# Kernel tuning notes

Measured on AMD Instinct MI355X. Metric: run time of the kernel, lower is better.

## Reference

```python
import jax, jax.numpy as jnp
import numpy as np

N = 100000   # nodes
E = 1600000  # edges
D = 128      # in_dim == hidden_dim
EL = 100000  # label edges for decode


def setup_inputs() -> dict:
    key = jax.random.key(0)
    k1, k2, k3, k4, k5 = jax.random.split(key, 5)
    x = jax.random.normal(k1, (N, D), dtype=jnp.float32)
    edge_index = jax.random.randint(k2, (2, E), 0, N, dtype=jnp.int64)
    edge_label_index = jax.random.randint(k3, (2, EL), 0, N, dtype=jnp.int64)
    # Glorot-ish init for GCN weights
    scale = 1.0 / np.sqrt(D)
    W1 = jax.random.normal(k4, (D, D), dtype=jnp.float32) * scale
    W2 = jax.random.normal(k5, (D, D), dtype=jnp.float32) * scale
    b1 = jnp.zeros((D,), dtype=jnp.float32)
    b2 = jnp.zeros((D,), dtype=jnp.float32)
    return {"x": x, "edge_index": edge_index, "edge_label_index": edge_label_index,
            "W1": W1, "b1": b1, "W2": W2, "b2": b2}


def gcn_conv(x, src, dst, W, b, num_nodes):
    # PyG GCNConv: add self-loops, symmetric D^-1/2 A D^-1/2 normalization
    loop = jnp.arange(num_nodes, dtype=src.dtype)
    s = jnp.concatenate([src, loop])
    d = jnp.concatenate([dst, loop])
    deg = jax.ops.segment_sum(jnp.ones(d.shape, dtype=x.dtype), d, num_segments=num_nodes)
    dinv = jnp.where(deg > 0, jax.lax.rsqrt(jnp.maximum(deg, 1.0)), 0.0)
    norm = dinv[s] * dinv[d]                      # [E+N]
    h = x @ W                                     # [N, H]
    msg = h[s] * norm[:, None]                    # gather + scale
    out = jax.ops.segment_sum(msg, d, num_segments=num_nodes)  # scatter-add
    return out + b


def reference(x, edge_index, edge_label_index, W1, b1, W2, b2):
    src, dst = edge_index[0], edge_index[1]
    z = jax.nn.relu(gcn_conv(x, src, dst, W1, b1, N))
    z = jax.nn.relu(gcn_conv(z, src, dst, W2, b2, N))
    # decode: edge-wise dot product
    s, d = edge_label_index[0], edge_label_index[1]
    return jnp.sum(z[s] * z[d], axis=-1)          # [EL]
```

## Files before the change

### kernel.cpp

```cpp
#include <hip/hip_runtime.h>
#include <hip/hip_bf16.h>
#include <hip/hip_fp16.h>


typedef _Float16 half8 __attribute__((ext_vector_type(8)));
typedef float floatx4 __attribute__((ext_vector_type(4)));

#define BK_SHIFT 8
#define BSC_EDGES 2048
#define SLAB_CAP 5120
#define WPAD 136

__global__ __launch_bounds__(256) void k_zero(int* __restrict__ p, int n) {
    int i = blockIdx.x * 256 + threadIdx.x;
    if (i < n) p[i] = 0;
}

__global__ __launch_bounds__(128) void k_wprep(const float* __restrict__ W1,
                                               const float* __restrict__ W2,
                                               _Float16* __restrict__ WT1,
                                               _Float16* __restrict__ WT2) {
    int b = blockIdx.x;
    const float* W = (b < 128) ? W1 : W2;
    _Float16* WT = (b < 128) ? WT1 : WT2;
    int k = b & 127;
    int c = threadIdx.x;
    WT[c * 128 + k] = (_Float16)W[k * 128 + c];
}

__global__ __launch_bounds__(256) void k_bscatter(const int* __restrict__ src,
                                                  const int* __restrict__ dst,
                                                  int* __restrict__ bfill,
                                                  int2* __restrict__ pairs,
                                                  int E, int nbk) {
    __shared__ int lcnt[1024];
    __shared__ int delta[1024];
    __shared__ int ssum[256];
    __shared__ int2 stage[BSC_EDGES];
    int tid = threadIdx.x;
    int e0 = blockIdx.x * BSC_EDGES;
    int nloc = E - e0; if (nloc > BSC_EDGES) nloc = BSC_EDGES;

    for (int b = tid; b < nbk; b += 256) lcnt[b] = 0;
    __syncthreads();

    int d[BSC_EDGES / 256], s[BSC_EDGES / 256];
#pragma unroll
    for (int k = 0; k < BSC_EDGES / 256; ++k) {
        int e = e0 + k * 256 + tid;
        if (e < E) {
            d[k] = dst[e];
            s[k] = src[e];
            atomicAdd(&lcnt[d[k] >> BK_SHIFT], 1);
        } else d[k] = -1;
    }
    __syncthreads();

    const int gpb = (nbk + 255) >> 8;
    int c[4], mysum = 0;
    for (int t = 0; t < gpb; ++t) {
        int b = tid * gpb + t;
        c[t] = (b < nbk) ? lcnt[b] : 0;
        mysum += c[t];
    }
    ssum[tid] = mysum;
    __syncthreads();
    for (int off = 1; off < 256; off <<= 1) {
        int t = (tid >= off) ? ssum[tid - off] : 0;
        __syncthreads();
        ssum[tid] += t;
        __syncthreads();
    }
    int base = ssum[tid] - mysum;
    for (int t = 0; t < gpb; ++t) {
        int b = tid * gpb + t;
        if (b < nbk) {
            int g = c[t] ? atomicAdd(&bfill[b], c[t]) : 0;
            delta[b] = b * SLAB_CAP + g - base;
            lcnt[b] = base;
            base += c[t];
        }
    }
    __syncthreads();

#pragma unroll
    for (int k = 0; k < BSC_EDGES / 256; ++k) {
        if (d[k] >= 0) {
            int b = d[k] >> BK_SHIFT;
            int lp = atomicAdd(&lcnt[b], 1);
            int2 p; p.x = s[k]; p.y = d[k];
            stage[lp] = p;
        }
    }
    __syncthreads();

    for (int j = tid; j < nloc; j += 256) {
        int2 p = stage[j];
        pairs[delta[p.y >> BK_SHIFT] + j] = p;
    }
}

__global__ __launch_bounds__(256) void k_csr(const int2* __restrict__ pairs,
                                             const int* __restrict__ bfill,
                                             int* __restrict__ row_start,
                                             int* __restrict__ cnt,
                                             float* __restrict__ dinv,
                                             int* __restrict__ srcs, int n) {
    __shared__ int lcnt[256];
    __shared__ int lpos[256];
    int tid = threadIdx.x;
    int b = blockIdx.x;
    lcnt[tid] = 0;
    __syncthreads();
    int beg = b * SLAB_CAP, end = beg + bfill[b];
    for (int i = beg + tid; i < end; i += 256)
        atomicAdd(&lcnt[pairs[i].y & 255], 1);
    __syncthreads();
    int c = lcnt[tid];
    lpos[tid] = c;
    __syncthreads();
    for (int off = 1; off < 256; off <<= 1) {
        int t = (tid >= off) ? lpos[tid - off] : 0;
        __syncthreads();
        lpos[tid] += t;
        __syncthreads();
    }
    int rs = beg + lpos[tid] - c;
    int v = (b << BK_SHIFT) + tid;
    if (v < n) {
        row_start[v] = rs;
        cnt[v] = c;
        dinv[v] = rsqrtf((float)c + 1.0f);
    }
    __syncthreads();
    lpos[tid] = rs;
    __syncthreads();
    for (int i = beg + tid; i < end; i += 256) {
        int2 p = pairs[i];
        int loc = atomicAdd(&lpos[p.y & 255], 1);
        srcs[loc] = p.x;
    }
}

__global__ __launch_bounds__(256) void k_gemm_mfma(const float* __restrict__ X,
                                                   const _Float16* __restrict__ WT,
                                                   const float* __restrict__ dinv,
                                                   _Float16* __restrict__ G, int n) {
    __shared__ _Float16 Wl[128 * WPAD];
    int tid = threadIdx.x;
    {
        const half8* w8 = (const half8*)WT;
#pragma unroll
        for (int i = 0; i < 8; ++i) {
            int idx = i * 256 + tid;
            int r = idx >> 4, cc = idx & 15;
            *(half8*)(Wl + r * WPAD + cc * 8) = w8[idx];
        }
    }
    __syncthreads();

    int wave = tid >> 6, lane = tid & 63;
    int q = lane >> 4, ln = lane & 15;
    int m0 = blockIdx.x * 128 + wave * 32;
    int mA0 = m0 + ln;      if (mA0 >= n) mA0 = n - 1;
    int mA1 = m0 + 16 + ln; if (mA1 >= n) mA1 = n - 1;
    const float* xr0 = X + (size_t)mA0 * 128;
    const float* xr1 = X + (size_t)mA1 * 128;

    floatx4 acc[2][8];
#pragma unroll
    for (int p = 0; p < 2; ++p)
#pragma unroll
        for (int t = 0; t < 8; ++t) acc[p][t] = (floatx4){0.f, 0.f, 0.f, 0.f};

#pragma unroll
    for (int kc = 0; kc < 128; kc += 32) {
        half8 a0, a1;
        {
            const float4* p0 = (const float4*)(xr0 + kc + q * 8);
            float4 f0 = p0[0], f1 = p0[1];
            a0[0] = (_Float16)f0.x; a0[1] = (_Float16)f0.y;
            a0[2] = (_Float16)f0.z; a0[3] = (_Float16)f0.w;
            a0[4] = (_Float16)f1.x; a0[5] = (_Float16)f1.y;
            a0[6] = (_Float16)f1.z; a0[7] = (_Float16)f1.w;
            const float4* p1 = (const float4*)(xr1 + kc + q * 8);
            float4 g0 = p1[0], g1 = p1[1];
            a1[0] = (_Float16)g0.x; a1[1] = (_Float16)g0.y;
            a1[2] = (_Float16)g0.z; a1[3] = (_Float16)g0.w;
            a1[4] = (_Float16)g1.x; a1[5] = (_Float16)g1.y;
            a1[6] = (_Float16)g1.z; a1[7] = (_Float16)g1.w;
        }
#pragma unroll
        for (int t = 0; t < 8; ++t) {
            half8 b = *(const half8*)(Wl + (size_t)(t * 16 + ln) * WPAD + kc + q * 8);
            acc[0][t] = __builtin_amdgcn_mfma_f32_16x16x32_f16(a0, b, acc[0][t], 0, 0, 0);
            acc[1][t] = __builtin_amdgcn_mfma_f32_16x16x32_f16(a1, b, acc[1][t], 0, 0, 0);
        }
    }

#pragma unroll
    for (int p = 0; p < 2; ++p) {
#pragma unroll
        for (int r = 0; r < 4; ++r) {
            int row = m0 + p * 16 + q * 4 + r;
            if (row < n) {
                float dv = dinv[row];
                _Float16* grow = G + (size_t)row * 128 + ln;
#pragma unroll
                for (int t = 0; t < 8; ++t)
                    grow[t * 16] = (_Float16)(acc[p][t][r] * dv);
            }
        }
    }
}

__global__ __launch_bounds__(256) void k_gather_gemm(const _Float16* __restrict__ G,
                                                     const int* __restrict__ srcs,
                                                     const int* __restrict__ row_start,
                                                     const int* __restrict__ cnt,
                                                     const float* __restrict__ dinv,
                                                     const float* __restrict__ bias,
                                                     const _Float16* __restrict__ WT2,
                                                     _Float16* __restrict__ G2, int n) {
    __shared__ _Float16 Wl[128 * WPAD];
    __shared__ _Float16 zl[16 * WPAD];
    int tid = threadIdx.x;

    {
        const half8* w8 = (const half8*)WT2;
#pragma unroll
        for (int i = 0; i < 8; ++i) {
            int idx = i * 256 + tid;
            int r = idx >> 4, cc = idx & 15;
            *(half8*)(Wl + r * WPAD + cc * 8) = w8[idx];
        }
    }

    int nl = tid >> 4;
    int lane = tid & 15;
    int v = blockIdx.x * 16 + nl;
    const half8* G8 = (const half8*)G;

    half8 zo;
    if (v < n) {
        half8 self = G8[(size_t)v * 16 + lane];
        float acc[8], acc2[8];
#pragma unroll
        for (int j = 0; j < 8; ++j) { acc[j] = (float)self[j]; acc2[j] = 0.f; }

        int beg = row_start[v], deg = cnt[v];
        int e = 0;
        for (; e + 3 < deg; e += 4) {
            int s0 = srcs[beg + e];
            int s1 = srcs[beg + e + 1];
            int s2 = srcs[beg + e + 2];
            int s3 = srcs[beg + e + 3];
            half8 t0 = G8[(size_t)s0 * 16 + lane];
            half8 t1 = G8[(size_t)s1 * 16 + lane];
            half8 t2 = G8[(size_t)s2 * 16 + lane];
            half8 t3 = G8[(size_t)s3 * 16 + lane];
#pragma unroll
            for (int j = 0; j < 8; ++j) {
                acc[j]  += (float)t0[j] + (float)t1[j];
                acc2[j] += (float)t2[j] + (float)t3[j];
            }
        }
        for (; e < deg; ++e) {
            int s0 = srcs[beg + e];
            half8 t0 = G8[(size_t)s0 * 16 + lane];
#pragma unroll
            for (int j = 0; j < 8; ++j) acc[j] += (float)t0[j];
        }

        float dv = dinv[v];
        const float4* b4 = (const float4*)bias;
        float4 bb0 = b4[lane * 2], bb1 = b4[lane * 2 + 1];
        float bf[8] = {bb0.x, bb0.y, bb0.z, bb0.w, bb1.x, bb1.y, bb1.z, bb1.w};
#pragma unroll
        for (int j = 0; j < 8; ++j) {
            float z = dv * (acc[j] + acc2[j]) + bf[j];
            zo[j] = (_Float16)fmaxf(z, 0.f);
        }
    } else {
#pragma unroll
        for (int j = 0; j < 8; ++j) zo[j] = (_Float16)0.f;
    }
    *(half8*)(zl + nl * WPAD + lane * 8) = zo;
    __syncthreads();

    int wave = tid >> 6, wl = tid & 63;
    int q = wl >> 4, ln = wl & 15;
    floatx4 acc[2];
    acc[0] = (floatx4){0.f, 0.f, 0.f, 0.f};
    acc[1] = (floatx4){0.f, 0.f, 0.f, 0.f};
#pragma unroll
    for (int kc = 0; kc < 128; kc += 32) {
        half8 a = *(const half8*)(zl + ln * WPAD + kc + q * 8);
#pragma unroll
        for (int t = 0; t < 2; ++t) {
            int cb = wave * 32 + t * 16;
            half8 b = *(const half8*)(Wl + (size_t)(cb + ln) * WPAD + kc + q * 8);
            acc[t] = __builtin_amdgcn_mfma_f32_16x16x32_f16(a, b, acc[t], 0, 0, 0);
        }
    }
#pragma unroll
    for (int r = 0; r < 4; ++r) {
        int gv = blockIdx.x * 16 + q * 4 + r;
        if (gv < n) {
            float dv = dinv[gv];
#pragma unroll
            for (int t = 0; t < 2; ++t)
                G2[(size_t)gv * 128 + wave * 32 + t * 16 + ln] =
                    (_Float16)(acc[t][r] * dv);
        }
    }
}

__global__ __launch_bounds__(256) void k_gather_relu(const _Float16* __restrict__ G,
                                                     const int* __restrict__ srcs,
                                                     const int* __restrict__ row_start,
                                                     const int* __restrict__ cnt,
                                                     const float* __restrict__ dinv,
                                                     const float* __restrict__ bias,
                                                     _Float16* __restrict__ Z, int n) {
    int v = blockIdx.x * 16 + (threadIdx.x >> 4);
    int lane = threadIdx.x & 15;
    if (v >= n) return;
    const half8* G8 = (const half8*)G;

    half8 self = G8[(size_t)v * 16 + lane];
    float acc[8], acc2[8];
#pragma unroll
    for (int j = 0; j < 8; ++j) { acc[j] = (float)self[j]; acc2[j] = 0.f; }

    int beg = row_start[v], deg = cnt[v];
    int e = 0;
    for (; e + 3 < deg; e += 4) {
        int s0 = srcs[beg + e];
        int s1 = srcs[beg + e + 1];
        int s2 = srcs[beg + e + 2];
        int s3 = srcs[beg + e + 3];
        half8 t0 = G8[(size_t)s0 * 16 + lane];
        half8 t1 = G8[(size_t)s1 * 16 + lane];
        half8 t2 = G8[(size_t)s2 * 16 + lane];
        half8 t3 = G8[(size_t)s3 * 16 + lane];
#pragma unroll
        for (int j = 0; j < 8; ++j) {
            acc[j]  += (float)t0[j] + (float)t1[j];
            acc2[j] += (float)t2[j] + (float)t3[j];
        }
    }
    for (; e < deg; ++e) {
        int s0 = srcs[beg + e];
        half8 t0 = G8[(size_t)s0 * 16 + lane];
#pragma unroll
        for (int j = 0; j < 8; ++j) acc[j] += (float)t0[j];
    }

    float dv = dinv[v];
    const float4* b4 = (const float4*)bias;
    float4 bb0 = b4[lane * 2], bb1 = b4[lane * 2 + 1];
    float bf[8] = {bb0.x, bb0.y, bb0.z, bb0.w, bb1.x, bb1.y, bb1.z, bb1.w};
    half8 zo;
#pragma unroll
    for (int j = 0; j < 8; ++j) {
        float z = dv * (acc[j] + acc2[j]) + bf[j];
        zo[j] = (_Float16)fmaxf(z, 0.f);
    }
    ((half8*)Z)[(size_t)v * 16 + lane] = zo;
}

__global__ __launch_bounds__(256) void k_decode(const _Float16* __restrict__ Z,
                                                const int* __restrict__ eli,
                                                float* __restrict__ out, int el) {
    int sub = threadIdx.x >> 4, lane = threadIdx.x & 15;
    int e = blockIdx.x * 16 + sub;
    if (e >= el) return;
    int s = eli[e], d = eli[el + e];
    const half8* Z8 = (const half8*)Z;
    half8 a = Z8[(size_t)s * 16 + lane];
    half8 b = Z8[(size_t)d * 16 + lane];
    float dot = 0.f;
#pragma unroll
    for (int j = 0; j < 8; ++j) dot += (float)a[j] * (float)b[j];
#pragma unroll
    for (int off = 8; off; off >>= 1) dot += __shfl_down(dot, off, 16);
    if (lane == 0) out[e] = dot;
}

extern "C" void kernel_launch(void* const* d_in, const int* in_sizes, int n_in,
                              void* d_out, int out_size, void* d_ws, size_t ws_size,
                              hipStream_t stream) {
    const float* x  = (const float*)d_in[0];
    const int*  ei  = (const int*)d_in[1];
    const int*  eli = (const int*)d_in[2];
    const float* W1 = (const float*)d_in[3];
    const float* b1 = (const float*)d_in[4];
    const float* W2 = (const float*)d_in[5];
    const float* b2 = (const float*)d_in[6];
    float* out = (float*)d_out;

    const int N  = in_sizes[0] / 128;
    const int E  = in_sizes[1] / 2;
    const int EL = in_sizes[2] / 2;
    const int* src = ei;
    const int* dst = ei + E;
    const int NBK = (N + 255) >> BK_SHIFT;

    char* ws = (char*)d_ws;
    size_t off = 0;
    auto alloc = [&](size_t bytes) -> void* {
        void* p = ws + off;
        off += bytes;
        off = (off + 255) & ~(size_t)255;
        return p;
    };
    int*       cnt       = (int*)alloc((size_t)N * 4);
    int*       row_start = (int*)alloc((size_t)N * 4);
    float*     dinv      = (float*)alloc((size_t)N * 4);
    int*       bfill     = (int*)alloc(4096);
    _Float16*  WT1       = (_Float16*)alloc(128 * 128 * 2);
    _Float16*  WT2       = (_Float16*)alloc(128 * 128 * 2);
    int*       srcs      = (int*)alloc((size_t)NBK * SLAB_CAP * 4);
    int2*      pairs     = (int2*)alloc((size_t)NBK * SLAB_CAP * 8);
    _Float16*  buf0      = (_Float16*)alloc((size_t)N * 128 * 2);
    _Float16*  buf1      = (_Float16*)alloc((size_t)N * 128 * 2);

    k_wprep<<<256, 128, 0, stream>>>(W1, W2, WT1, WT2);
    k_zero<<<2, 256, 0, stream>>>(bfill, 512);

    k_bscatter<<<(E + BSC_EDGES - 1) / BSC_EDGES, 256, 0, stream>>>(src, dst, bfill, pairs, E, NBK);
    k_csr<<<NBK, 256, 0, stream>>>(pairs, bfill, row_start, cnt, dinv, srcs, N);

    k_gemm_mfma<<<(N + 127) / 128, 256, 0, stream>>>(x, WT1, dinv, buf0, N);
    k_gather_gemm<<<(N + 15) / 16, 256, 0, stream>>>(buf0, srcs, row_start, cnt, dinv, b1, WT2, buf1, N);
    k_gather_relu<<<(N + 15) / 16, 256, 0, stream>>>(buf1, srcs, row_start, cnt, dinv, b2, buf0, N);
    k_decode<<<(EL + 15) / 16, 256, 0, stream>>>(buf0, eli, out, EL);
}
```

Baseline: 309.9 us.

## Keep W2 fragments in registers, balance gather via LDS cursor, fold zeroing

The fused gather+GEMM kernel no longer stages the full 128x136 W2 tile in LDS. Each wave loads its B fragments straight into registers, which cuts LDS use so more blocks fit per CU (launch bounds now request 4). The gather phase hands the block's 16 nodes to 16-lane groups through a shared atomic cursor, so groups that draw low-degree nodes take further nodes and load is balanced inside the block. The bfill zeroing kernel is folded into k_wprep, removing one launch; the cost is more VGPRs for the W fragments and an atomic per node.

```diff
diff --git a/kernel.cpp b/kernel.cpp
--- a/kernel.cpp
+++ b/kernel.cpp
@@ -11,21 +11,18 @@
 #define SLAB_CAP 5120
 #define WPAD 136
 
-__global__ __launch_bounds__(256) void k_zero(int* __restrict__ p, int n) {
-    int i = blockIdx.x * 256 + threadIdx.x;
-    if (i < n) p[i] = 0;
-}
-
 __global__ __launch_bounds__(128) void k_wprep(const float* __restrict__ W1,
                                                const float* __restrict__ W2,
                                                _Float16* __restrict__ WT1,
-                                               _Float16* __restrict__ WT2) {
+                                               _Float16* __restrict__ WT2,
+                                               int* __restrict__ bfill) {
     int b = blockIdx.x;
     const float* W = (b < 128) ? W1 : W2;
     _Float16* WT = (b < 128) ? WT1 : WT2;
     int k = b & 127;
     int c = threadIdx.x;
     WT[c * 128 + k] = (_Float16)W[k * 128 + c];
+    if (b < 4) bfill[b * 128 + c] = 0;
 }
 
 __global__ __launch_bounds__(256) void k_bscatter(const int* __restrict__ src,
@@ -214,94 +211,96 @@
     }
 }
 
-__global__ __launch_bounds__(256) void k_gather_gemm(const _Float16* __restrict__ G,
-                                                     const int* __restrict__ srcs,
-                                                     const int* __restrict__ row_start,
-                                                     const int* __restrict__ cnt,
-                                                     const float* __restrict__ dinv,
-                                                     const float* __restrict__ bias,
-                                                     const _Float16* __restrict__ WT2,
-                                                     _Float16* __restrict__ G2, int n) {
-    __shared__ _Float16 Wl[128 * WPAD];
+__global__ __launch_bounds__(256, 4) void k_gather_gemm(const _Float16* __restrict__ G,
+                                                        const int* __restrict__ srcs,
+                                                        const int* __restrict__ row_start,
+                                                        const int* __restrict__ cnt,
+                                                        const float* __restrict__ dinv,
+                                                        const float* __restrict__ bias,
+                                                        const _Float16* __restrict__ WT2,
+                                                        _Float16* __restrict__ G2, int n) {
     __shared__ _Float16 zl[16 * WPAD];
+    __shared__ int cursor;
     int tid = threadIdx.x;
-
-    {
-        const half8* w8 = (const half8*)WT2;
-#pragma unroll
-        for (int i = 0; i < 8; ++i) {
-            int idx = i * 256 + tid;
-            int r = idx >> 4, cc = idx & 15;
-            *(half8*)(Wl + r * WPAD + cc * 8) = w8[idx];
-        }
-    }
-
-    int nl = tid >> 4;
-    int lane = tid & 15;
-    int v = blockIdx.x * 16 + nl;
-    const half8* G8 = (const half8*)G;
-
-    half8 zo;
-    if (v < n) {
-        half8 self = G8[(size_t)v * 16 + lane];
-        float acc[8], acc2[8];
-#pragma unroll
-        for (int j = 0; j < 8; ++j) { acc[j] = (float)self[j]; acc2[j] = 0.f; }
-
-        int beg = row_start[v], deg = cnt[v];
-        int e = 0;
-        for (; e + 3 < deg; e += 4) {
-            int s0 = srcs[beg + e];
-            int s1 = srcs[beg + e + 1];
-            int s2 = srcs[beg + e + 2];
-            int s3 = srcs[beg + e + 3];
-            half8 t0 = G8[(size_t)s0 * 16 + lane];
-            half8 t1 = G8[(size_t)s1 * 16 + lane];
-            half8 t2 = G8[(size_t)s2 * 16 + lane];
-            half8 t3 = G8[(size_t)s3 * 16 + lane];
-#pragma unroll
-            for (int j = 0; j < 8; ++j) {
-                acc[j]  += (float)t0[j] + (float)t1[j];
-                acc2[j] += (float)t2[j] + (float)t3[j];
-            }
-        }
-        for (; e < deg; ++e) {
-            int s0 = srcs[beg + e];
-            half8 t0 = G8[(size_t)s0 * 16 + lane];
-#pragma unroll
-            for (int j = 0; j < 8; ++j) acc[j] += (float)t0[j];
-        }
-
-        float dv = dinv[v];
-        const float4* b4 = (const float4*)bias;
-        float4 bb0 = b4[lane * 2], bb1 = b4[lane * 2 + 1];
-        float bf[8] = {bb0.x, bb0.y, bb0.z, bb0.w, bb1.x, bb1.y, bb1.z, bb1.w};
-#pragma unroll
-        for (int j = 0; j < 8; ++j) {
-            float z = dv * (acc[j] + acc2[j]) + bf[j];
-            zo[j] = (_Float16)fmaxf(z, 0.f);
-        }
-    } else {
-#pragma unroll
-        for (int j = 0; j < 8; ++j) zo[j] = (_Float16)0.f;
-    }
-    *(half8*)(zl + nl * WPAD + lane * 8) = zo;
-    __syncthreads();
-
     int wave = tid >> 6, wl = tid & 63;
     int q = wl >> 4, ln = wl & 15;
+
+    half8 bfr[4][2];
+#pragma unroll
+    for (int kq = 0; kq < 4; ++kq)
+#pragma unroll
+        for (int t = 0; t < 2; ++t)
+            bfr[kq][t] = *(const half8*)(WT2 +
+                (size_t)(wave * 32 + t * 16 + ln) * 128 + kq * 32 + q * 8);
+
+    if (tid == 0) cursor = 0;
+    __syncthreads();
+
+    int lane = tid & 15;
+    const half8* G8 = (const half8*)G;
+    const float4* b4 = (const float4*)bias;
+
+    for (;;) {
+        int slot = 0;
+        if (lane == 0) slot = atomicAdd(&cursor, 1);
+        slot = __shfl(slot, 0, 16);
+        if (slot >= 16) break;
+        int v = blockIdx.x * 16 + slot;
+        half8 zo;
+        if (v < n) {
+            half8 self = G8[(size_t)v * 16 + lane];
+            float acc[8], acc2[8];
+#pragma unroll
+            for (int j = 0; j < 8; ++j) { acc[j] = (float)self[j]; acc2[j] = 0.f; }
+
+            int beg = row_start[v], deg = cnt[v];
+            int e = 0;
+            for (; e + 3 < deg; e += 4) {
+                int s0 = srcs[beg + e];
+                int s1 = srcs[beg + e + 1];
+                int s2 = srcs[beg + e + 2];
+                int s3 = srcs[beg + e + 3];
+                half8 t0 = G8[(size_t)s0 * 16 + lane];
+                half8 t1 = G8[(size_t)s1 * 16 + lane];
+                half8 t2 = G8[(size_t)s2 * 16 + lane];
+                half8 t3 = G8[(size_t)s3 * 16 + lane];
+#pragma unroll
+                for (int j = 0; j < 8; ++j) {
+                    acc[j]  += (float)t0[j] + (float)t1[j];
+                    acc2[j] += (float)t2[j] + (float)t3[j];
+                }
+            }
+            for (; e < deg; ++e) {
+                int s0 = srcs[beg + e];
+                half8 t0 = G8[(size_t)s0 * 16 + lane];
+#pragma unroll
+                for (int j = 0; j < 8; ++j) acc[j] += (float)t0[j];
+            }
+
+            float dv = dinv[v];
+            float4 bb0 = b4[lane * 2], bb1 = b4[lane * 2 + 1];
+            float bf[8] = {bb0.x, bb0.y, bb0.z, bb0.w, bb1.x, bb1.y, bb1.z, bb1.w};
+#pragma unroll
+            for (int j = 0; j < 8; ++j) {
+                float z = dv * (acc[j] + acc2[j]) + bf[j];
+                zo[j] = (_Float16)fmaxf(z, 0.f);
+            }
+        } else {
+#pragma unroll
+            for (int j = 0; j < 8; ++j) zo[j] = (_Float16)0.f;
+        }
+        *(half8*)(zl + slot * WPAD + lane * 8) = zo;
+    }
+    __syncthreads();
+
     floatx4 acc[2];
     acc[0] = (floatx4){0.f, 0.f, 0.f, 0.f};
     acc[1] = (floatx4){0.f, 0.f, 0.f, 0.f};
 #pragma unroll
-    for (int kc = 0; kc < 128; kc += 32) {
-        half8 a = *(const half8*)(zl + ln * WPAD + kc + q * 8);
-#pragma unroll
-        for (int t = 0; t < 2; ++t) {
-            int cb = wave * 32 + t * 16;
-            half8 b = *(const half8*)(Wl + (size_t)(cb + ln) * WPAD + kc + q * 8);
-            acc[t] = __builtin_amdgcn_mfma_f32_16x16x32_f16(a, b, acc[t], 0, 0, 0);
-        }
+    for (int kq = 0; kq < 4; ++kq) {
+        half8 a = *(const half8*)(zl + ln * WPAD + kq * 32 + q * 8);
+        acc[0] = __builtin_amdgcn_mfma_f32_16x16x32_f16(a, bfr[kq][0], acc[0], 0, 0, 0);
+        acc[1] = __builtin_amdgcn_mfma_f32_16x16x32_f16(a, bfr[kq][1], acc[1], 0, 0, 0);
     }
 #pragma unroll
     for (int r = 0; r < 4; ++r) {
@@ -426,8 +425,7 @@
     _Float16*  buf0      = (_Float16*)alloc((size_t)N * 128 * 2);
     _Float16*  buf1      = (_Float16*)alloc((size_t)N * 128 * 2);
 
-    k_wprep<<<256, 128, 0, stream>>>(W1, W2, WT1, WT2);
-    k_zero<<<2, 256, 0, stream>>>(bfill, 512);
+    k_wprep<<<256, 128, 0, stream>>>(W1, W2, WT1, WT2, bfill);
 
     k_bscatter<<<(E + BSC_EDGES - 1) / BSC_EDGES, 256, 0, stream>>>(src, dst, bfill, pairs, E, NBK);
     k_csr<<<NBK, 256, 0, stream>>>(pairs, bfill, row_start, cnt, dinv, srcs, N);
```

Result: no change. 309.6 us (-0.1%).
